# Kernel optimization log

Hardware: AMD Instinct MI355X
Metric: run time of the kernel (lower is better)

The kernel has to match this reference:

```python
import jax, jax.numpy as jnp
import numpy as np

B, T, D = 2, 2048, 2048
H, HD = 16, 128          # n_heads, head_dim (D = H * HD)
THETA = 10000.0
TOPK_RATIO = 0.55
EPS = 1e-5


def _ste(x, q):
    # straight-through estimator: forward = q, backward = identity
    return x + jax.lax.stop_gradient(q - x)


def ternary_weight(w):
    # absmean ternary quantization to {-1, 0, +1} * scale
    scale = jnp.mean(jnp.abs(w))
    wq = jnp.clip(jnp.round(w / (scale + EPS)), -1.0, 1.0) * scale
    return _ste(w, wq)


def quant_int(x, bits):
    # per-token (last-dim) absmax quantization to signed `bits`-bit grid
    qmax = 2.0 ** (bits - 1) - 1.0
    s = qmax / jnp.clip(jnp.max(jnp.abs(x), axis=-1, keepdims=True), EPS, None)
    q = jnp.clip(jnp.round(x * s), -qmax - 1.0, qmax) / s
    return _ste(x, q)


def topk_sparsify(x, ratio):
    # keep top-k values by magnitude per token, zero the rest
    d = x.shape[-1]
    k = max(1, int(ratio * d))
    flat = x.reshape(-1, d)
    _, idx = jax.lax.top_k(jnp.abs(flat), k)
    mask = jnp.zeros_like(flat).at[jnp.arange(flat.shape[0])[:, None], idx].set(1.0)
    return (flat * _ste(jnp.ones_like(flat), mask)).reshape(x.shape)


def bitlinear(x, w, act_mode):
    if act_mode == 'int4':
        x = quant_int(x, 4)
    elif act_mode == 'topk_int8':
        x = quant_int(topk_sparsify(x, TOPK_RATIO), 8)
    return x @ ternary_weight(w).T


def rope(x):
    # x: (B, H, T, hd); rotate-half RoPE with cat([freqs, freqs]) layout
    hd, t = x.shape[-1], x.shape[2]
    inv = 1.0 / THETA ** (jnp.arange(0, hd, 2, dtype=jnp.float32) / hd)
    freqs = jnp.arange(t, dtype=jnp.float32)[:, None] * inv[None, :]  # (T, hd/2)
    emb = jnp.concatenate([freqs, freqs], axis=-1)                     # (T, hd)
    cos = jnp.cos(emb)[None, None]
    sin = jnp.sin(emb)[None, None]
    x1, x2 = x[..., : hd // 2], x[..., hd // 2 :]
    rot = jnp.concatenate([-x2, x1], axis=-1)
    return x * cos + rot * sin


def setup_inputs() -> dict:
    key = jax.random.key(0)
    ks = jax.random.split(key, 5)
    return {
        'x': jax.random.normal(ks[0], (B, T, D), dtype=jnp.float32),
        'wq': jax.random.normal(ks[1], (D, D), dtype=jnp.float32) * 0.02,
        'wk': jax.random.normal(ks[2], (D, D), dtype=jnp.float32) * 0.02,
        'wv': jax.random.normal(ks[3], (D, D), dtype=jnp.float32) * 0.02,
        'wo': jax.random.normal(ks[4], (D, D), dtype=jnp.float32) * 0.02,
    }


def reference(x, wq, wk, wv, wo):
    b, t, _ = x.shape
    q = bitlinear(x, wq, 'int4').reshape(b, t, H, HD).transpose(0, 2, 1, 3)
    k = bitlinear(x, wk, 'int4').reshape(b, t, H, HD).transpose(0, 2, 1, 3)
    v = bitlinear(x, wv, 'int4').reshape(b, t, H, HD).transpose(0, 2, 1, 3)
    q = rope(q)
    k = rope(k)
    # bidirectional SDPA, no mask
    scores = jnp.einsum('bhqd,bhkd->bhqk', q, k) / jnp.sqrt(jnp.float32(HD))
    attn = jax.nn.softmax(scores, axis=-1)
    out = jnp.einsum('bhqk,bhkd->bhqd', attn, v)
    out = out.transpose(0, 2, 1, 3).reshape(b, t, H * HD)
    return bitlinear(out, wo, 'topk_int8')
```

## Files before the change

### kernel.cpp

```cpp
#include <hip/hip_runtime.h>
#include <stdint.h>
#include <math.h>


typedef __attribute__((ext_vector_type(8))) short short8;
typedef __attribute__((ext_vector_type(4))) int i32x4;
typedef __attribute__((ext_vector_type(8))) _Float16 f16x8;
typedef __attribute__((ext_vector_type(16))) float f32x16;

#define GLDS16(g, l)                                                        \
  __builtin_amdgcn_global_load_lds(                                         \
      (const __attribute__((address_space(1))) void*)(g),                   \
      (__attribute__((address_space(3))) void*)(l), 16, 0, 0)

__device__ __forceinline__ unsigned short f2bf(float v) {
  return (unsigned short)(__float_as_uint(v) >> 16);
}

__global__ __launch_bounds__(256) void k_costab(float* __restrict__ ct,
                                                float* __restrict__ st) {
  int idx = blockIdx.x * 256 + threadIdx.x;
  int t = idx >> 6, i = idx & 63;
  float f = (float)(2 * i) / 128.0f;
  float inv = 1.0f / powf(10000.0f, f);
  float fr = (float)t * inv;
  ct[idx] = cosf(fr);
  st[idx] = sinf(fr);
}

__global__ __launch_bounds__(256) void k_wsum(const float* __restrict__ w0,
                                              const float* __restrict__ w1,
                                              const float* __restrict__ w2,
                                              const float* __restrict__ w3,
                                              double* __restrict__ part) {
  int bx = blockIdx.x;
  int mat = bx >> 10;
  const float* w = (mat == 0) ? w0 : (mat == 1) ? w1 : (mat == 2) ? w2 : w3;
  int base = (bx & 1023) * 4096;
  double s = 0.0;
#pragma unroll
  for (int i = 0; i < 16; ++i)
    s += (double)fabsf(w[base + threadIdx.x + i * 256]);
  __shared__ double red[256];
  red[threadIdx.x] = s;
  __syncthreads();
  for (int off = 128; off; off >>= 1) {
    if (threadIdx.x < off) red[threadIdx.x] += red[threadIdx.x + off];
    __syncthreads();
  }
  if (threadIdx.x == 0) part[bx] = red[0];
}

__global__ __launch_bounds__(256) void k_wscale(const double* __restrict__ part,
                                                float* __restrict__ wsc) {
  int m = blockIdx.x, tid = threadIdx.x;
  const double* p = part + m * 1024;
  double s = p[tid] + p[tid + 256] + p[tid + 512] + p[tid + 768];
  __shared__ double red[256];
  red[tid] = s;
  __syncthreads();
  for (int off = 128; off; off >>= 1) {
    if (tid < off) red[tid] += red[tid + off];
    __syncthreads();
  }
  if (tid == 0) wsc[m] = (float)(red[0] / 4194304.0);
}

__global__ __launch_bounds__(256) void k_wquant(const float* __restrict__ w0,
                                                const float* __restrict__ w1,
                                                const float* __restrict__ w2,
                                                const float* __restrict__ w3,
                                                const float* __restrict__ wsc,
                                                signed char* __restrict__ wt) {
  int mat = blockIdx.y;
  const float* w = (mat == 0) ? w0 : (mat == 1) ? w1 : (mat == 2) ? w2 : w3;
  float se = wsc[mat] + 1e-5f;
  size_t base = (size_t)blockIdx.x * 4096;
  signed char* o = wt + (size_t)mat * 4194304 + base;
  const float* wp = w + base;
#pragma unroll 4
  for (int i = 0; i < 16; ++i) {
    int idx = threadIdx.x + i * 256;
    float v = rintf(wp[idx] / se);
    v = fminf(fmaxf(v, -1.0f), 1.0f);
    o[idx] = (signed char)v;
  }
}

__global__ __launch_bounds__(256) void k_xquant(const float* __restrict__ x,
                                                signed char* __restrict__ xq,
                                                float* __restrict__ sx) {
  int row = blockIdx.x, tid = threadIdx.x;
  const float* xr = x + (size_t)row * 2048;
  float v[8];
  float mx = 0.0f;
#pragma unroll
  for (int i = 0; i < 8; ++i) {
    v[i] = xr[tid + i * 256];
    mx = fmaxf(mx, fabsf(v[i]));
  }
  __shared__ float red[256];
  red[tid] = mx;
  __syncthreads();
  for (int off = 128; off; off >>= 1) {
    if (tid < off) red[tid] = fmaxf(red[tid], red[tid + off]);
    __syncthreads();
  }
  float s = 7.0f / fmaxf(red[0], 1e-5f);
#pragma unroll
  for (int i = 0; i < 8; ++i) {
    float q = rintf(v[i] * s);
    q = fminf(fmaxf(q, -8.0f), 7.0f);
    xq[(size_t)row * 2048 + tid + i * 256] = (signed char)q;
  }
  if (tid == 0) sx[row] = s;
}

__global__ __launch_bounds__(256) void k_gemm3(const signed char* __restrict__ A,
                                               const signed char* __restrict__ wtall,
                                               float* __restrict__ qo,
                                               float* __restrict__ vo,
                                               _Float16* __restrict__ khp,
                                               _Float16* __restrict__ klp,
                                               const float* __restrict__ srow,
                                               const float* __restrict__ wsc,
                                               const float* __restrict__ ct,
                                               const float* __restrict__ st) {
  __shared__ alignas(16) signed char As[128 * 64];
  __shared__ alignas(16) signed char Bs[128 * 64];
  __shared__ float fac[128];
  const int tid = threadIdx.x, wave = tid >> 6, lane = tid & 63;
  const int bxi = blockIdx.x;
  const int mat = bxi >> 4;
  const signed char* Bw = wtall + (size_t)mat * 4194304;
  const int brow = blockIdx.y * 128, bcol = (bxi & 15) * 128;
  if (tid < 128) fac[tid] = wsc[mat] / srow[brow + tid];
  const int wr = wave >> 1, wc = wave & 1;
  i32x4 acc[4][4];
#pragma unroll
  for (int m = 0; m < 4; ++m)
#pragma unroll
    for (int n = 0; n < 4; ++n) acc[m][n] = (i32x4){0, 0, 0, 0};
  const int srl = tid >> 2;
  const int ssw = ((tid & 3) ^ ((srl >> 1) & 3)) * 16;
  const signed char* Ag = A + (size_t)(brow + srl) * 2048 + ssw;
  const signed char* Bg = Bw + (size_t)(bcol + srl) * 2048 + ssw;
  char* AsB = (char*)As + wave * 1024;
  char* BsB = (char*)Bs + wave * 1024;
  const int fr = lane & 15, kb = lane >> 4;
  const int rsl = (kb ^ ((fr >> 1) & 3)) * 16;
  for (int k0 = 0; k0 < 2048; k0 += 64) {
    __syncthreads();
    GLDS16(Ag + k0, AsB);
    GLDS16(Ag + k0 + (size_t)64 * 2048, AsB + 4096);
    GLDS16(Bg + k0, BsB);
    GLDS16(Bg + k0 + (size_t)64 * 2048, BsB + 4096);
    __syncthreads();
    i32x4 af[4], bf[4];
#pragma unroll
    for (int m = 0; m < 4; ++m)
      af[m] = *(const i32x4*)&As[(wr * 64 + m * 16 + fr) * 64 + rsl];
#pragma unroll
    for (int n = 0; n < 4; ++n)
      bf[n] = *(const i32x4*)
           &Bs[(wc * 32 + (n & 1) * 16 + (n >> 1) * 64 + fr) * 64 + rsl];
#pragma unroll
    for (int m = 0; m < 4; ++m)
#pragma unroll
      for (int n = 0; n < 4; ++n)
        acc[m][n] = __builtin_amdgcn_mfma_i32_16x16x64_i8(af[m], bf[n],
                                                          acc[m][n], 0, 0, 0);
  }
  const int fq = lane >> 4;
  if (mat == 2) {
#pragma unroll
    for (int m = 0; m < 4; ++m)
#pragma unroll
      for (int n = 0; n < 4; ++n) {
        int col = bcol + wc * 32 + (n & 1) * 16 + (n >> 1) * 64 + fr;
#pragma unroll
        for (int r = 0; r < 4; ++r) {
          int row = wr * 64 + m * 16 + fq * 4 + r;
          vo[(size_t)(brow + row) * 2048 + col] = (float)acc[m][n][r] * fac[row];
        }
      }
  } else {
    const int hh = bcol >> 7;
#pragma unroll
    for (int m = 0; m < 4; ++m)
#pragma unroll
      for (int n = 0; n < 2; ++n) {
        int d1 = wc * 32 + n * 16 + fr;
#pragma unroll
        for (int r = 0; r < 4; ++r) {
          int row = wr * 64 + m * 16 + fq * 4 + r;
          int rg = brow + row;
          int t = rg & 2047, bb = rg >> 11;
          float c = ct[t * 64 + d1], sn = st[t * 64 + d1];
          float x1 = (float)acc[m][n][r] * fac[row];
          float x2 = (float)acc[m][n + 2][r] * fac[row];
          float y1 = x1 * c - x2 * sn;
          float y2 = x2 * c + x1 * sn;
          if (mat == 0) {
            qo[(size_t)rg * 2048 + bcol + d1] = y1;
            qo[(size_t)rg * 2048 + bcol + d1 + 64] = y2;
          } else {
            size_t ob = ((size_t)(bb * 16 + hh) * 2048 + t) * 128 + d1;
            _Float16 h1 = (_Float16)y1, h2 = (_Float16)y2;
            khp[ob] = h1;
            khp[ob + 64] = h2;
            klp[ob] = (_Float16)(y1 - (float)h1);
            klp[ob + 64] = (_Float16)(y2 - (float)h2);
          }
        }
      }
  }
}

__global__ __launch_bounds__(256) void k_gemm(const signed char* __restrict__ A,
                                              const signed char* __restrict__ Bw,
                                              float* __restrict__ C,
                                              const float* __restrict__ srow,
                                              const float* __restrict__ wsp) {
  __shared__ alignas(16) signed char As[128 * 64];
  __shared__ alignas(16) signed char Bs[128 * 64];
  __shared__ float fac[128];
  const int tid = threadIdx.x, wave = tid >> 6, lane = tid & 63;
  const int brow = blockIdx.y * 128, bcol = blockIdx.x * 128;
  if (tid < 128) fac[tid] = wsp[0] / srow[brow + tid];
  const int wr = wave >> 1, wc = wave & 1;
  i32x4 acc[4][4];
#pragma unroll
  for (int m = 0; m < 4; ++m)
#pragma unroll
    for (int n = 0; n < 4; ++n) acc[m][n] = (i32x4){0, 0, 0, 0};
  const int srl = tid >> 2;
  const int ssw = ((tid & 3) ^ ((srl >> 1) & 3)) * 16;
  const signed char* Ag = A + (size_t)(brow + srl) * 2048 + ssw;
  const signed char* Bg = Bw + (size_t)(bcol + srl) * 2048 + ssw;
  char* AsB = (char*)As + wave * 1024;
  char* BsB = (char*)Bs + wave * 1024;
  const int fr = lane & 15, kb = lane >> 4;
  const int rsl = (kb ^ ((fr >> 1) & 3)) * 16;
  for (int k0 = 0; k0 < 2048; k0 += 64) {
    __syncthreads();
    GLDS16(Ag + k0, AsB);
    GLDS16(Ag + k0 + (size_t)64 * 2048, AsB + 4096);
    GLDS16(Bg + k0, BsB);
    GLDS16(Bg + k0 + (size_t)64 * 2048, BsB + 4096);
    __syncthreads();
    i32x4 af[4], bf[4];
#pragma unroll
    for (int m = 0; m < 4; ++m)
      af[m] = *(const i32x4*)&As[(wr * 64 + m * 16 + fr) * 64 + rsl];
#pragma unroll
    for (int n = 0; n < 4; ++n)
      bf[n] = *(const i32x4*)&Bs[(wc * 64 + n * 16 + fr) * 64 + rsl];
#pragma unroll
    for (int m = 0; m < 4; ++m)
#pragma unroll
      for (int n = 0; n < 4; ++n)
        acc[m][n] = __builtin_amdgcn_mfma_i32_16x16x64_i8(af[m], bf[n],
                                                          acc[m][n], 0, 0, 0);
  }
  const int fq = lane >> 4;
#pragma unroll
  for (int m = 0; m < 4; ++m)
#pragma unroll
    for (int n = 0; n < 4; ++n)
#pragma unroll
      for (int r = 0; r < 4; ++r) {
        int row = wr * 64 + m * 16 + fq * 4 + r;
        C[(size_t)(brow + row) * 2048 + bcol + wc * 64 + n * 16 + fr] =
            (float)acc[m][n][r] * fac[row];
      }
}

__global__ __launch_bounds__(256) void k_vtrans(const float* __restrict__ vb,
                                                _Float16* __restrict__ vth,
                                                _Float16* __restrict__ vtl) {
  __shared__ float F[64][133];
  const int tid = threadIdx.x;
  const int bh = blockIdx.y, b = bh >> 4, h = bh & 15;
  const int t0 = blockIdx.x * 64;
  {
    const int tr = tid >> 2, tc = (tid & 3) * 32;
    const float* src = vb + ((size_t)(b * 2048 + t0 + tr)) * 2048 + h * 128 + tc;
#pragma unroll
    for (int j = 0; j < 8; ++j) {
      float4 v = *(const float4*)(src + j * 4);
      F[tr][tc + j * 4 + 0] = v.x;
      F[tr][tc + j * 4 + 1] = v.y;
      F[tr][tc + j * 4 + 2] = v.z;
      F[tr][tc + j * 4 + 3] = v.w;
    }
  }
  __syncthreads();
  {
    const int vd = tid >> 1, th = (tid & 1) * 32;
    f16x8 oh[4], ol[4];
#pragma unroll
    for (int j = 0; j < 32; ++j) {
      float x = F[th + j][vd];
      _Float16 hv = (_Float16)x;
      oh[j >> 3][j & 7] = hv;
      ol[j >> 3][j & 7] = (_Float16)(x - (float)hv);
    }
    _Float16* dh = vth + ((size_t)bh * 128 + vd) * 2048 + t0 + th;
    _Float16* dl = vtl + ((size_t)bh * 128 + vd) * 2048 + t0 + th;
#pragma unroll
    for (int j4 = 0; j4 < 4; ++j4) {
      *(f16x8*)(dh + j4 * 8) = oh[j4];
      *(f16x8*)(dl + j4 * 8) = ol[j4];
    }
  }
}

__global__ __launch_bounds__(256, 2) void k_attn(float* __restrict__ qb,
                                                 const _Float16* __restrict__ kh,
                                                 const _Float16* __restrict__ kl,
                                                 const _Float16* __restrict__ vth,
                                                 const _Float16* __restrict__ vtl) {
  __shared__ alignas(16) char KS[2][2][32 * 256];
  __shared__ alignas(16) char VS[2][2][128 * 64];
  const int tid = threadIdx.x;
  const int wave = tid >> 6, lane = tid & 63;
  const int rl = lane & 31, hi = lane >> 5, hi8 = hi * 8;
  const int bid = blockIdx.x;
  const int xcd = bid & 7, li = bid >> 3;
  const int bh = xcd * 4 + (li >> 4), qt = li & 15;
  const int b = bh >> 4, h = bh & 15;
  const size_t rowbase = (size_t)b * 2048;
  const int hcol = h * 128;
  const float F = 0.08838834764831845f * 1.44269504088896f;
  const float THR = 11.5415603f;

  f16x8 qh[8], ql[8];
  {
    const float* qsrc =
        qb + (rowbase + qt * 128 + wave * 32 + rl) * 2048 + hcol + hi8;
#pragma unroll
    for (int ds = 0; ds < 8; ++ds) {
      float4 a = *(const float4*)(qsrc + ds * 16);
      float4 c = *(const float4*)(qsrc + ds * 16 + 4);
      float v[8] = {a.x, a.y, a.z, a.w, c.x, c.y, c.z, c.w};
      f16x8 hh, ll;
#pragma unroll
      for (int i = 0; i < 8; ++i) {
        float sv = v[i] * F;
        _Float16 hv = (_Float16)sv;
        hh[i] = hv;
        ll[i] = (_Float16)(sv - (float)hv);
      }
      qh[ds] = hh;
      ql[ds] = ll;
    }
  }

  const int krl = lane >> 4, ksl = lane & 15;
  const int vrl = lane >> 2, vsl = lane & 3;
  size_t kofs[2], vofs[2];
#pragma unroll
  for (int i = 0; i < 2; ++i) {
    int krow = wave * 8 + i * 4 + krl;
    kofs[i] = (size_t)krow * 128 + ((ksl ^ (krow & 7)) << 3);
    int vrow = wave * 32 + i * 16 + vrl;
    vofs[i] = (size_t)vrow * 2048 + ((vsl ^ (vrow & 3)) << 3);
  }
  const _Float16* gkh = kh + (size_t)bh * 262144;
  const _Float16* gkl = kl + (size_t)bh * 262144;
  const _Float16* gvh = vth + (size_t)bh * 262144;
  const _Float16* gvl = vtl + (size_t)bh * 262144;

  f32x16 Oa[4];
#pragma unroll
  for (int df = 0; df < 4; ++df)
#pragma unroll
    for (int i = 0; i < 16; ++i) Oa[df][i] = 0.0f;
  float m = -INFINITY, lsum = 0.0f;

  {
#pragma unroll
    for (int i = 0; i < 2; ++i) {
      GLDS16(gkh + kofs[i], KS[0][0] + wave * 2048 + i * 1024);
      GLDS16(gkl + kofs[i], KS[0][1] + wave * 2048 + i * 1024);
      GLDS16(gvh + vofs[i], VS[0][0] + wave * 2048 + i * 1024);
      GLDS16(gvl + vofs[i], VS[0][1] + wave * 2048 + i * 1024);
    }
  }

  for (int kt = 0; kt < 64; ++kt) {
    const int bf = kt & 1;
    __syncthreads();
    if (kt < 63) {
      const _Float16* pkh = gkh + (size_t)(kt + 1) * 4096;
      const _Float16* pkl = gkl + (size_t)(kt + 1) * 4096;
      const _Float16* pvh = gvh + (size_t)(kt + 1) * 32;
      const _Float16* pvl = gvl + (size_t)(kt + 1) * 32;
      char* kd0 = KS[bf ^ 1][0] + wave * 2048;
      char* kd1 = KS[bf ^ 1][1] + wave * 2048;
      char* vd0 = VS[bf ^ 1][0] + wave * 2048;
      char* vd1 = VS[bf ^ 1][1] + wave * 2048;
#pragma unroll
      for (int i = 0; i < 2; ++i) {
        GLDS16(pkh + kofs[i], kd0 + i * 1024);
        GLDS16(pkl + kofs[i], kd1 + i * 1024);
        GLDS16(pvh + vofs[i], vd0 + i * 1024);
        GLDS16(pvl + vofs[i], vd1 + i * 1024);
      }
    }
    f32x16 sA = {}, sB = {}, sC = {};
    __builtin_amdgcn_s_setprio(1);
#pragma unroll
    for (int ds = 0; ds < 8; ++ds) {
      const int ra = rl * 256 + (((2 * ds + hi) ^ (rl & 7)) << 4);
      f16x8 ah = *(const f16x8*)(KS[bf][0] + ra);
      f16x8 al = *(const f16x8*)(KS[bf][1] + ra);
      sA = __builtin_amdgcn_mfma_f32_32x32x16_f16(ah, qh[ds], sA, 0, 0, 0);
      sB = __builtin_amdgcn_mfma_f32_32x32x16_f16(ah, ql[ds], sB, 0, 0, 0);
      sC = __builtin_amdgcn_mfma_f32_32x32x16_f16(al, qh[ds], sC, 0, 0, 0);
    }
    __builtin_amdgcn_s_setprio(0);
    f32x16 s;
#pragma unroll
    for (int i = 0; i < 16; ++i) s[i] = (sA[i] + sB[i]) + sC[i];
    float pm = fmaxf(
        fmaxf(fmaxf(fmaxf(s[0], s[1]), fmaxf(s[2], s[3])),
              fmaxf(fmaxf(s[4], s[5]), fmaxf(s[6], s[7]))),
        fmaxf(fmaxf(fmaxf(s[8], s[9]), fmaxf(s[10], s[11])),
              fmaxf(fmaxf(s[12], s[13]), fmaxf(s[14], s[15]))));
    pm = fmaxf(pm, __shfl_xor(pm, 32));
    float alpha = 1.0f;
    if (__any(pm > m + THR)) {
      float mn = fmaxf(m, pm);
      alpha = exp2f(m - mn);
      m = mn;
#pragma unroll
      for (int reg = 0; reg < 16; ++reg) {
        int qr = (reg & 3) + 8 * (reg >> 2) + 4 * hi;
        float av = __shfl(alpha, qr);
        Oa[0][reg] *= av;
        Oa[1][reg] *= av;
        Oa[2][reg] *= av;
        Oa[3][reg] *= av;
      }
    }
    unsigned int pkhh[4][2], pkll[4][2];
    float ls = 0.0f;
#pragma unroll
    for (int t4 = 0; t4 < 4; ++t4)
#pragma unroll
      for (int c2 = 0; c2 < 2; ++c2) {
        float pa = exp2f(s[4 * t4 + 2 * c2] - m);
        float pb = exp2f(s[4 * t4 + 2 * c2 + 1] - m);
        ls += pa + pb;
        auto hp = __builtin_amdgcn_cvt_pkrtz(pa, pb);
        float la = pa - (float)hp[0], lb = pb - (float)hp[1];
        auto lp = __builtin_amdgcn_cvt_pkrtz(la, lb);
        pkhh[t4][c2] = __builtin_bit_cast(unsigned int, hp);
        pkll[t4][c2] = __builtin_bit_cast(unsigned int, lp);
      }
    ls += __shfl_xor(ls, 32);
    lsum = lsum * alpha + ls;
    f16x8 paH[2], paL[2];
#pragma unroll
    for (int hf = 0; hf < 2; ++hf) {
      {
        unsigned int a0 = pkhh[2 * hf][0], b0 = pkhh[2 * hf + 1][0];
        unsigned int a1 = pkhh[2 * hf][1], b1 = pkhh[2 * hf + 1][1];
        asm("v_permlane32_swap_b32 %0, %1" : "+v"(a0), "+v"(b0));
        asm("v_permlane32_swap_b32 %0, %1" : "+v"(a1), "+v"(b1));
        uint4 u;
        u.x = a0; u.y = a1; u.z = b0; u.w = b1;
        paH[hf] = __builtin_bit_cast(f16x8, u);
      }
      {
        unsigned int a0 = pkll[2 * hf][0], b0 = pkll[2 * hf + 1][0];
        unsigned int a1 = pkll[2 * hf][1], b1 = pkll[2 * hf + 1][1];
        asm("v_permlane32_swap_b32 %0, %1" : "+v"(a0), "+v"(b0));
        asm("v_permlane32_swap_b32 %0, %1" : "+v"(a1), "+v"(b1));
        uint4 u;
        u.x = a0; u.y = a1; u.z = b0; u.w = b1;
        paL[hf] = __builtin_bit_cast(f16x8, u);
      }
    }
    __builtin_amdgcn_s_setprio(1);
#pragma unroll
    for (int df = 0; df < 4; ++df) {
#pragma unroll
      for (int hf = 0; hf < 2; ++hf) {
        const int va = (df * 32 + rl) * 64 + (((2 * hf + hi) ^ (rl & 3)) << 4);
        f16x8 vh = *(const f16x8*)(VS[bf][0] + va);
        f16x8 vl = *(const f16x8*)(VS[bf][1] + va);
        Oa[df] = __builtin_amdgcn_mfma_f32_32x32x16_f16(paH[hf], vh, Oa[df], 0, 0, 0);
        Oa[df] = __builtin_amdgcn_mfma_f32_32x32x16_f16(paH[hf], vl, Oa[df], 0, 0, 0);
        Oa[df] = __builtin_amdgcn_mfma_f32_32x32x16_f16(paL[hf], vh, Oa[df], 0, 0, 0);
      }
    }
    __builtin_amdgcn_s_setprio(0);
  }
  float linv = 1.0f / lsum;
  float* obase = qb + (rowbase + qt * 128 + wave * 32) * 2048 + hcol;
#pragma unroll
  for (int reg = 0; reg < 16; ++reg) {
    int qr = (reg & 3) + 8 * (reg >> 2) + 4 * hi;
    float lv = __shfl(linv, qr);
    float* orow = obase + (size_t)qr * 2048;
    orow[0 * 32 + rl] = Oa[0][reg] * lv;
    orow[1 * 32 + rl] = Oa[1][reg] * lv;
    orow[2 * 32 + rl] = Oa[2][reg] * lv;
    orow[3 * 32 + rl] = Oa[3][reg] * lv;
  }
}

__global__ __launch_bounds__(256) void k_topk(const float* __restrict__ ain,
                                              signed char* __restrict__ oq,
                                              float* __restrict__ so) {
  const int row = blockIdx.x, tid = threadIdx.x;
  const float* xr = ain + (size_t)row * 2048;
  __shared__ unsigned int bits[2048];
  __shared__ unsigned int hist[256];
  __shared__ unsigned int scn[256];
  __shared__ unsigned int stat[3];
#pragma unroll
  for (int j = 0; j < 8; ++j) {
    int i = tid * 8 + j;
    bits[i] = __float_as_uint(xr[i]) & 0x7fffffffu;
  }
  unsigned int mx = 0;
#pragma unroll
  for (int j = 0; j < 8; ++j) mx = max(mx, bits[tid * 8 + j]);
  scn[tid] = mx;
  __syncthreads();
  for (int off = 128; off; off >>= 1) {
    if (tid < off) scn[tid] = max(scn[tid], scn[tid + off]);
    __syncthreads();
  }
  if (tid == 0) { stat[0] = 0u; stat[1] = 1126u; stat[2] = scn[0]; }
  for (int p = 0; p < 4; ++p) {
    const int shift = 24 - 8 * p;
    hist[tid] = 0u;
    __syncthreads();
    unsigned int pref = stat[0];
    unsigned int rk0 = stat[1];
#pragma unroll
    for (int j = 0; j < 8; ++j) {
      unsigned int u = bits[tid * 8 + j];
      bool match = (p == 0) || ((u >> (shift + 8)) == pref);
      if (match) atomicAdd(&hist[(u >> shift) & 255u], 1u);
    }
    __syncthreads();
    scn[tid] = hist[tid];
    __syncthreads();
    for (int off = 1; off < 256; off <<= 1) {
      unsigned int v = (tid + off < 256) ? scn[tid + off] : 0u;
      __syncthreads();
      scn[tid] += v;
      __syncthreads();
    }
    unsigned int nxt = (tid == 255) ? 0u : scn[tid + 1];
    if (scn[tid] >= rk0 && nxt < rk0) {
      stat[0] = (pref << 8) | (unsigned int)tid;
      stat[1] = rk0 - nxt;
    }
    __syncthreads();
  }
  const unsigned int T = stat[0];
  const unsigned int rkeep = stat[1];
  const float rowmax = __uint_as_float(stat[2]);
  const float s = 127.0f / fmaxf(rowmax, 1e-5f);
  unsigned int cnt = 0;
#pragma unroll
  for (int j = 0; j < 8; ++j) cnt += (bits[tid * 8 + j] == T) ? 1u : 0u;
  scn[tid] = cnt;
  __syncthreads();
  for (int off = 1; off < 256; off <<= 1) {
    unsigned int v = (tid >= off) ? scn[tid - off] : 0u;
    __syncthreads();
    scn[tid] += v;
    __syncthreads();
  }
  unsigned int eqr = scn[tid] - cnt;
#pragma unroll
  for (int j = 0; j < 8; ++j) {
    int i = tid * 8 + j;
    unsigned int u = bits[i];
    bool keep = u > T;
    if (u == T) { keep = (eqr < rkeep); eqr++; }
    float q = 0.0f;
    if (keep) {
      q = rintf(xr[i] * s);
      q = fminf(fmaxf(q, -128.0f), 127.0f);
    }
    oq[(size_t)row * 2048 + i] = (signed char)q;
  }
  if (tid == 0) so[row] = s;
}

extern "C" void kernel_launch(void* const* d_in, const int* in_sizes, int n_in,
                              void* d_out, int out_size, void* d_ws,
                              size_t ws_size, hipStream_t stream) {
  const float* x = (const float*)d_in[0];
  const float* wq = (const float*)d_in[1];
  const float* wk = (const float*)d_in[2];
  const float* wv = (const float*)d_in[3];
  const float* wo = (const float*)d_in[4];
  float* out = (float*)d_out;

  char* ws = (char*)d_ws;
  size_t off = 0;
  auto alloc = [&](size_t bytes) -> void* {
    void* p = ws + off;
    off += (bytes + 255) & ~(size_t)255;
    return p;
  };
  signed char* wt = (signed char*)alloc(4ull * 2048 * 2048);
  signed char* xq = (signed char*)alloc(4096ull * 2048);
  float* qb = (float*)alloc(4096ull * 2048 * 4);
  float* vb = (float*)alloc(4096ull * 2048 * 4);
  _Float16* kh = (_Float16*)alloc(32ull * 2048 * 128 * 2);
  _Float16* kl = (_Float16*)alloc(32ull * 2048 * 128 * 2);
  _Float16* vth = (_Float16*)alloc(32ull * 128 * 2048 * 2);
  _Float16* vtl = (_Float16*)alloc(32ull * 128 * 2048 * 2);
  float* ct = (float*)alloc(2048ull * 64 * 4);
  float* st = (float*)alloc(2048ull * 64 * 4);
  float* sx = (float*)alloc(4096 * 4);
  float* so = (float*)alloc(4096 * 4);
  float* wsc = (float*)alloc(4 * 4);
  double* prt = (double*)alloc(4096 * 8);
  signed char* oq = (signed char*)vb;

  k_costab<<<512, 256, 0, stream>>>(ct, st);
  k_wsum<<<4096, 256, 0, stream>>>(wq, wk, wv, wo, prt);
  k_wscale<<<4, 256, 0, stream>>>(prt, wsc);
  k_wquant<<<dim3(1024, 4), 256, 0, stream>>>(wq, wk, wv, wo, wsc, wt);
  k_xquant<<<4096, 256, 0, stream>>>(x, xq, sx);

  k_gemm3<<<dim3(48, 32), 256, 0, stream>>>(xq, wt, qb, vb, kh, kl, sx, wsc,
                                            ct, st);
  k_vtrans<<<dim3(32, 32), 256, 0, stream>>>(vb, vth, vtl);
  k_attn<<<512, 256, 0, stream>>>(qb, kh, kl, vth, vtl);
  k_topk<<<4096, 256, 0, stream>>>(qb, oq, so);
  k_gemm<<<dim3(16, 32), 256, 0, stream>>>(oq, wt + 3ull * 4194304, out, so,
                                           wsc + 3);
}
```

Baseline: 442.3 us.

## Fuse V transpose into projection GEMM and software-pipeline attention PV step

The V projection epilogue now converts results to split fp16 hi/lo and writes them already transposed through shared memory, so the separate k_vtrans kernel and the fp32 V buffer round trip are no longer needed. In the attention kernel, the softmax and PV MFMAs for the previous key tile now run while the current tile's QK^T scores are computed. V tiles are loaded one iteration later, and a final drain step after the loop handles the last tile. This adds extra shared-memory syncs in the GEMM epilogue and keeps more scores live in registers, which may raise register pressure in the attention kernel.

```diff
diff --git a/kernel.cpp b/kernel.cpp
--- a/kernel.cpp
+++ b/kernel.cpp
@@ -119,9 +119,10 @@
 __global__ __launch_bounds__(256) void k_gemm3(const signed char* __restrict__ A,
                                                const signed char* __restrict__ wtall,
                                                float* __restrict__ qo,
-                                               float* __restrict__ vo,
                                                _Float16* __restrict__ khp,
                                                _Float16* __restrict__ klp,
+                                               _Float16* __restrict__ vth,
+                                               _Float16* __restrict__ vtl,
                                                const float* __restrict__ srow,
                                                const float* __restrict__ wsc,
                                                const float* __restrict__ ct,
@@ -172,20 +173,43 @@
                                                           acc[m][n], 0, 0, 0);
   }
   const int fq = lane >> 4;
+  const int hh = bcol >> 7;
+  const int bb0 = brow >> 11, tbase = brow & 2047;
   if (mat == 2) {
-#pragma unroll
-    for (int m = 0; m < 4; ++m)
-#pragma unroll
-      for (int n = 0; n < 4; ++n) {
-        int col = bcol + wc * 32 + (n & 1) * 16 + (n >> 1) * 64 + fr;
-#pragma unroll
-        for (int r = 0; r < 4; ++r) {
-          int row = wr * 64 + m * 16 + fq * 4 + r;
-          vo[(size_t)(brow + row) * 2048 + col] = (float)acc[m][n][r] * fac[row];
-        }
-      }
+    _Float16* Ah = (_Float16*)As;
+    _Float16* Al = (_Float16*)Bs;
+    const int bh = bb0 * 16 + hh;
+#pragma unroll
+    for (int q = 0; q < 4; ++q) {
+      __syncthreads();
+      if (wc == (q & 1)) {
+#pragma unroll
+        for (int m = 0; m < 4; ++m)
+#pragma unroll
+          for (int nn = 0; nn < 2; ++nn) {
+            int n = (q >> 1) * 2 + nn;
+            int dl = nn * 16 + fr;
+#pragma unroll
+            for (int r = 0; r < 4; ++r) {
+              int tl = wr * 64 + m * 16 + fq * 4 + r;
+              float val = (float)acc[m][n][r] * fac[tl];
+              _Float16 hv = (_Float16)val;
+              Ah[dl * 128 + tl] = hv;
+              Al[dl * 128 + tl] = (_Float16)(val - (float)hv);
+            }
+          }
+      }
+      __syncthreads();
+      {
+        int d = tid >> 3, tseg = (tid & 7) * 16;
+        size_t ob = ((size_t)bh * 128 + q * 32 + d) * 2048 + tbase + tseg;
+        *(f16x8*)(vth + ob) = *(const f16x8*)&Ah[d * 128 + tseg];
+        *(f16x8*)(vth + ob + 8) = *(const f16x8*)&Ah[d * 128 + tseg + 8];
+        *(f16x8*)(vtl + ob) = *(const f16x8*)&Al[d * 128 + tseg];
+        *(f16x8*)(vtl + ob + 8) = *(const f16x8*)&Al[d * 128 + tseg + 8];
+      }
+    }
   } else {
-    const int hh = bcol >> 7;
 #pragma unroll
     for (int m = 0; m < 4; ++m)
 #pragma unroll
@@ -195,7 +219,7 @@
         for (int r = 0; r < 4; ++r) {
           int row = wr * 64 + m * 16 + fq * 4 + r;
           int rg = brow + row;
-          int t = rg & 2047, bb = rg >> 11;
+          int t = rg & 2047;
           float c = ct[t * 64 + d1], sn = st[t * 64 + d1];
           float x1 = (float)acc[m][n][r] * fac[row];
           float x2 = (float)acc[m][n + 2][r] * fac[row];
@@ -205,7 +229,7 @@
             qo[(size_t)rg * 2048 + bcol + d1] = y1;
             qo[(size_t)rg * 2048 + bcol + d1 + 64] = y2;
           } else {
-            size_t ob = ((size_t)(bb * 16 + hh) * 2048 + t) * 128 + d1;
+            size_t ob = ((size_t)(bb0 * 16 + hh) * 2048 + t) * 128 + d1;
             _Float16 h1 = (_Float16)y1, h2 = (_Float16)y2;
             khp[ob] = h1;
             khp[ob + 64] = h2;
@@ -274,46 +298,6 @@
         C[(size_t)(brow + row) * 2048 + bcol + wc * 64 + n * 16 + fr] =
             (float)acc[m][n][r] * fac[row];
       }
-}
-
-__global__ __launch_bounds__(256) void k_vtrans(const float* __restrict__ vb,
-                                                _Float16* __restrict__ vth,
-                                                _Float16* __restrict__ vtl) {
-  __shared__ float F[64][133];
-  const int tid = threadIdx.x;
-  const int bh = blockIdx.y, b = bh >> 4, h = bh & 15;
-  const int t0 = blockIdx.x * 64;
-  {
-    const int tr = tid >> 2, tc = (tid & 3) * 32;
-    const float* src = vb + ((size_t)(b * 2048 + t0 + tr)) * 2048 + h * 128 + tc;
-#pragma unroll
-    for (int j = 0; j < 8; ++j) {
-      float4 v = *(const float4*)(src + j * 4);
-      F[tr][tc + j * 4 + 0] = v.x;
-      F[tr][tc + j * 4 + 1] = v.y;
-      F[tr][tc + j * 4 + 2] = v.z;
-      F[tr][tc + j * 4 + 3] = v.w;
-    }
-  }
-  __syncthreads();
-  {
-    const int vd = tid >> 1, th = (tid & 1) * 32;
-    f16x8 oh[4], ol[4];
-#pragma unroll
-    for (int j = 0; j < 32; ++j) {
-      float x = F[th + j][vd];
-      _Float16 hv = (_Float16)x;
-      oh[j >> 3][j & 7] = hv;
-      ol[j >> 3][j & 7] = (_Float16)(x - (float)hv);
-    }
-    _Float16* dh = vth + ((size_t)bh * 128 + vd) * 2048 + t0 + th;
-    _Float16* dl = vtl + ((size_t)bh * 128 + vd) * 2048 + t0 + th;
-#pragma unroll
-    for (int j4 = 0; j4 < 4; ++j4) {
-      *(f16x8*)(dh + j4 * 8) = oh[j4];
-      *(f16x8*)(dl + j4 * 8) = ol[j4];
-    }
-  }
 }
 
 __global__ __launch_bounds__(256, 2) void k_attn(float* __restrict__ qb,
@@ -378,15 +362,12 @@
 #pragma unroll
     for (int i = 0; i < 16; ++i) Oa[df][i] = 0.0f;
   float m = -INFINITY, lsum = 0.0f;
-
-  {
-#pragma unroll
-    for (int i = 0; i < 2; ++i) {
-      GLDS16(gkh + kofs[i], KS[0][0] + wave * 2048 + i * 1024);
-      GLDS16(gkl + kofs[i], KS[0][1] + wave * 2048 + i * 1024);
-      GLDS16(gvh + vofs[i], VS[0][0] + wave * 2048 + i * 1024);
-      GLDS16(gvl + vofs[i], VS[0][1] + wave * 2048 + i * 1024);
-    }
+  f32x16 sPrev;
+
+#pragma unroll
+  for (int i = 0; i < 2; ++i) {
+    GLDS16(gkh + kofs[i], KS[0][0] + wave * 2048 + i * 1024);
+    GLDS16(gkl + kofs[i], KS[0][1] + wave * 2048 + i * 1024);
   }
 
   for (int kt = 0; kt < 64; ++kt) {
@@ -395,16 +376,21 @@
     if (kt < 63) {
       const _Float16* pkh = gkh + (size_t)(kt + 1) * 4096;
       const _Float16* pkl = gkl + (size_t)(kt + 1) * 4096;
-      const _Float16* pvh = gvh + (size_t)(kt + 1) * 32;
-      const _Float16* pvl = gvl + (size_t)(kt + 1) * 32;
       char* kd0 = KS[bf ^ 1][0] + wave * 2048;
       char* kd1 = KS[bf ^ 1][1] + wave * 2048;
-      char* vd0 = VS[bf ^ 1][0] + wave * 2048;
-      char* vd1 = VS[bf ^ 1][1] + wave * 2048;
 #pragma unroll
       for (int i = 0; i < 2; ++i) {
         GLDS16(pkh + kofs[i], kd0 + i * 1024);
         GLDS16(pkl + kofs[i], kd1 + i * 1024);
+      }
+    }
+    {
+      const _Float16* pvh = gvh + (size_t)kt * 32;
+      const _Float16* pvl = gvl + (size_t)kt * 32;
+      char* vd0 = VS[bf][0] + wave * 2048;
+      char* vd1 = VS[bf][1] + wave * 2048;
+#pragma unroll
+      for (int i = 0; i < 2; ++i) {
         GLDS16(pvh + vofs[i], vd0 + i * 1024);
         GLDS16(pvl + vofs[i], vd1 + i * 1024);
       }
@@ -421,14 +407,96 @@
       sC = __builtin_amdgcn_mfma_f32_32x32x16_f16(al, qh[ds], sC, 0, 0, 0);
     }
     __builtin_amdgcn_s_setprio(0);
-    f32x16 s;
-#pragma unroll
-    for (int i = 0; i < 16; ++i) s[i] = (sA[i] + sB[i]) + sC[i];
+    if (kt > 0) {
+      const int pbf = (kt - 1) & 1;
+      float pm = fmaxf(
+          fmaxf(fmaxf(fmaxf(sPrev[0], sPrev[1]), fmaxf(sPrev[2], sPrev[3])),
+                fmaxf(fmaxf(sPrev[4], sPrev[5]), fmaxf(sPrev[6], sPrev[7]))),
+          fmaxf(fmaxf(fmaxf(sPrev[8], sPrev[9]), fmaxf(sPrev[10], sPrev[11])),
+                fmaxf(fmaxf(sPrev[12], sPrev[13]),
+                      fmaxf(sPrev[14], sPrev[15]))));
+      pm = fmaxf(pm, __shfl_xor(pm, 32));
+      float alpha = 1.0f;
+      if (__any(pm > m + THR)) {
+        float mn = fmaxf(m, pm);
+        alpha = exp2f(m - mn);
+        m = mn;
+#pragma unroll
+        for (int reg = 0; reg < 16; ++reg) {
+          int qr = (reg & 3) + 8 * (reg >> 2) + 4 * hi;
+          float av = __shfl(alpha, qr);
+          Oa[0][reg] *= av;
+          Oa[1][reg] *= av;
+          Oa[2][reg] *= av;
+          Oa[3][reg] *= av;
+        }
+      }
+      unsigned int pkhh[4][2], pkll[4][2];
+      float ls = 0.0f;
+#pragma unroll
+      for (int t4 = 0; t4 < 4; ++t4)
+#pragma unroll
+        for (int c2 = 0; c2 < 2; ++c2) {
+          float pa = exp2f(sPrev[4 * t4 + 2 * c2] - m);
+          float pb = exp2f(sPrev[4 * t4 + 2 * c2 + 1] - m);
+          ls += pa + pb;
+          auto hp = __builtin_amdgcn_cvt_pkrtz(pa, pb);
+          float la = pa - (float)hp[0], lb = pb - (float)hp[1];
+          auto lp = __builtin_amdgcn_cvt_pkrtz(la, lb);
+          pkhh[t4][c2] = __builtin_bit_cast(unsigned int, hp);
+          pkll[t4][c2] = __builtin_bit_cast(unsigned int, lp);
+        }
+      ls += __shfl_xor(ls, 32);
+      lsum = lsum * alpha + ls;
+      f16x8 paH[2], paL[2];
+#pragma unroll
+      for (int hf = 0; hf < 2; ++hf) {
+        {
+          unsigned int a0 = pkhh[2 * hf][0], b0 = pkhh[2 * hf + 1][0];
+          unsigned int a1 = pkhh[2 * hf][1], b1 = pkhh[2 * hf + 1][1];
+          asm("v_permlane32_swap_b32 %0, %1" : "+v"(a0), "+v"(b0));
+          asm("v_permlane32_swap_b32 %0, %1" : "+v"(a1), "+v"(b1));
+          uint4 u;
+          u.x = a0; u.y = a1; u.z = b0; u.w = b1;
+          paH[hf] = __builtin_bit_cast(f16x8, u);
+        }
+        {
+          unsigned int a0 = pkll[2 * hf][0], b0 = pkll[2 * hf + 1][0];
+          unsigned int a1 = pkll[2 * hf][1], b1 = pkll[2 * hf + 1][1];
+          asm("v_permlane32_swap_b32 %0, %1" : "+v"(a0), "+v"(b0));
+          asm("v_permlane32_swap_b32 %0, %1" : "+v"(a1), "+v"(b1));
+          uint4 u;
+          u.x = a0; u.y = a1; u.z = b0; u.w = b1;
+          paL[hf] = __builtin_bit_cast(f16x8, u);
+        }
+      }
+      __builtin_amdgcn_s_setprio(1);
+#pragma unroll
+      for (int df = 0; df < 4; ++df) {
+#pragma unroll
+        for (int hf = 0; hf < 2; ++hf) {
+          const int va =
+              (df * 32 + rl) * 64 + (((2 * hf + hi) ^ (rl & 3)) << 4);
+          f16x8 vh = *(const f16x8*)(VS[pbf][0] + va);
+          f16x8 vl = *(const f16x8*)(VS[pbf][1] + va);
+          Oa[df] = __builtin_amdgcn_mfma_f32_32x32x16_f16(paH[hf], vh, Oa[df], 0, 0, 0);
+          Oa[df] = __builtin_amdgcn_mfma_f32_32x32x16_f16(paH[hf], vl, Oa[df], 0, 0, 0);
+          Oa[df] = __builtin_amdgcn_mfma_f32_32x32x16_f16(paL[hf], vh, Oa[df], 0, 0, 0);
+        }
+      }
+      __builtin_amdgcn_s_setprio(0);
+    }
+#pragma unroll
+    for (int i = 0; i < 16; ++i) sPrev[i] = (sA[i] + sB[i]) + sC[i];
+  }
+  __syncthreads();
+  {
     float pm = fmaxf(
-        fmaxf(fmaxf(fmaxf(s[0], s[1]), fmaxf(s[2], s[3])),
-              fmaxf(fmaxf(s[4], s[5]), fmaxf(s[6], s[7]))),
-        fmaxf(fmaxf(fmaxf(s[8], s[9]), fmaxf(s[10], s[11])),
-              fmaxf(fmaxf(s[12], s[13]), fmaxf(s[14], s[15]))));
+        fmaxf(fmaxf(fmaxf(sPrev[0], sPrev[1]), fmaxf(sPrev[2], sPrev[3])),
+              fmaxf(fmaxf(sPrev[4], sPrev[5]), fmaxf(sPrev[6], sPrev[7]))),
+        fmaxf(fmaxf(fmaxf(sPrev[8], sPrev[9]), fmaxf(sPrev[10], sPrev[11])),
+              fmaxf(fmaxf(sPrev[12], sPrev[13]),
+                    fmaxf(sPrev[14], sPrev[15]))));
     pm = fmaxf(pm, __shfl_xor(pm, 32));
     float alpha = 1.0f;
     if (__any(pm > m + THR)) {
@@ -451,8 +519,8 @@
     for (int t4 = 0; t4 < 4; ++t4)
 #pragma unroll
       for (int c2 = 0; c2 < 2; ++c2) {
-        float pa = exp2f(s[4 * t4 + 2 * c2] - m);
-        float pb = exp2f(s[4 * t4 + 2 * c2 + 1] - m);
+        float pa = exp2f(sPrev[4 * t4 + 2 * c2] - m);
+        float pb = exp2f(sPrev[4 * t4 + 2 * c2 + 1] - m);
         ls += pa + pb;
         auto hp = __builtin_amdgcn_cvt_pkrtz(pa, pb);
         float la = pa - (float)hp[0], lb = pb - (float)hp[1];
@@ -484,20 +552,18 @@
         paL[hf] = __builtin_bit_cast(f16x8, u);
       }
     }
-    __builtin_amdgcn_s_setprio(1);
 #pragma unroll
     for (int df = 0; df < 4; ++df) {
 #pragma unroll
       for (int hf = 0; hf < 2; ++hf) {
         const int va = (df * 32 + rl) * 64 + (((2 * hf + hi) ^ (rl & 3)) << 4);
-        f16x8 vh = *(const f16x8*)(VS[bf][0] + va);
-        f16x8 vl = *(const f16x8*)(VS[bf][1] + va);
+        f16x8 vh = *(const f16x8*)(VS[1][0] + va);
+        f16x8 vl = *(const f16x8*)(VS[1][1] + va);
         Oa[df] = __builtin_amdgcn_mfma_f32_32x32x16_f16(paH[hf], vh, Oa[df], 0, 0, 0);
         Oa[df] = __builtin_amdgcn_mfma_f32_32x32x16_f16(paH[hf], vl, Oa[df], 0, 0, 0);
         Oa[df] = __builtin_amdgcn_mfma_f32_32x32x16_f16(paL[hf], vh, Oa[df], 0, 0, 0);
       }
     }
-    __builtin_amdgcn_s_setprio(0);
   }
   float linv = 1.0f / lsum;
   float* obase = qb + (rowbase + qt * 128 + wave * 32) * 2048 + hcol;
@@ -617,7 +683,7 @@
   signed char* wt = (signed char*)alloc(4ull * 2048 * 2048);
   signed char* xq = (signed char*)alloc(4096ull * 2048);
   float* qb = (float*)alloc(4096ull * 2048 * 4);
-  float* vb = (float*)alloc(4096ull * 2048 * 4);
+  signed char* oq = (signed char*)alloc(4096ull * 2048);
   _Float16* kh = (_Float16*)alloc(32ull * 2048 * 128 * 2);
   _Float16* kl = (_Float16*)alloc(32ull * 2048 * 128 * 2);
   _Float16* vth = (_Float16*)alloc(32ull * 128 * 2048 * 2);
@@ -628,7 +694,6 @@
   float* so = (float*)alloc(4096 * 4);
   float* wsc = (float*)alloc(4 * 4);
   double* prt = (double*)alloc(4096 * 8);
-  signed char* oq = (signed char*)vb;
 
   k_costab<<<512, 256, 0, stream>>>(ct, st);
   k_wsum<<<4096, 256, 0, stream>>>(wq, wk, wv, wo, prt);
@@ -636,9 +701,8 @@
   k_wquant<<<dim3(1024, 4), 256, 0, stream>>>(wq, wk, wv, wo, wsc, wt);
   k_xquant<<<4096, 256, 0, stream>>>(x, xq, sx);
 
-  k_gemm3<<<dim3(48, 32), 256, 0, stream>>>(xq, wt, qb, vb, kh, kl, sx, wsc,
-                                            ct, st);
-  k_vtrans<<<dim3(32, 32), 256, 0, stream>>>(vb, vth, vtl);
+  k_gemm3<<<dim3(48, 32), 256, 0, stream>>>(xq, wt, qb, kh, kl, vth, vtl, sx,
+                                            wsc, ct, st);
   k_attn<<<512, 256, 0, stream>>>(qb, kh, kl, vth, vtl);
   k_topk<<<4096, 256, 0, stream>>>(qb, oq, so);
   k_gemm<<<dim3(16, 32), 256, 0, stream>>>(oq, wt + 3ull * 4194304, out, so,
```

Result: faster. 428.2 us (-3.2%).

## Fuse V transpose into QKV GEMM and split attention over KV halves

Applied to the files above, without the earlier changes.

The V projection epilogue now writes transposed hi/lo fp16 V through shared memory, so the separate k_vtrans kernel and the fp32 V buffer are gone. Attention is split into two KV halves per query tile (1024 blocks, single-buffered LDS, higher occupancy bound). Each half writes unnormalised partial outputs plus m/l, and a new combine kernel merges them. This trades the removed transpose pass and the extra parallelism against extra partial-output traffic, a combine launch, and the loss of double-buffered K/V prefetch.

```diff
diff --git a/kernel.cpp b/kernel.cpp
--- a/kernel.cpp
+++ b/kernel.cpp
@@ -119,9 +119,10 @@
 __global__ __launch_bounds__(256) void k_gemm3(const signed char* __restrict__ A,
                                                const signed char* __restrict__ wtall,
                                                float* __restrict__ qo,
-                                               float* __restrict__ vo,
                                                _Float16* __restrict__ khp,
                                                _Float16* __restrict__ klp,
+                                               _Float16* __restrict__ vth,
+                                               _Float16* __restrict__ vtl,
                                                const float* __restrict__ srow,
                                                const float* __restrict__ wsc,
                                                const float* __restrict__ ct,
@@ -172,20 +173,43 @@
                                                           acc[m][n], 0, 0, 0);
   }
   const int fq = lane >> 4;
+  const int hh = bcol >> 7;
+  const int bb0 = brow >> 11, tbase = brow & 2047;
   if (mat == 2) {
-#pragma unroll
-    for (int m = 0; m < 4; ++m)
-#pragma unroll
-      for (int n = 0; n < 4; ++n) {
-        int col = bcol + wc * 32 + (n & 1) * 16 + (n >> 1) * 64 + fr;
-#pragma unroll
-        for (int r = 0; r < 4; ++r) {
-          int row = wr * 64 + m * 16 + fq * 4 + r;
-          vo[(size_t)(brow + row) * 2048 + col] = (float)acc[m][n][r] * fac[row];
-        }
-      }
+    _Float16* Ah = (_Float16*)As;
+    _Float16* Al = (_Float16*)Bs;
+    const int bh = bb0 * 16 + hh;
+#pragma unroll
+    for (int q = 0; q < 4; ++q) {
+      __syncthreads();
+      if (wc == (q & 1)) {
+#pragma unroll
+        for (int m = 0; m < 4; ++m)
+#pragma unroll
+          for (int nn = 0; nn < 2; ++nn) {
+            int n = (q >> 1) * 2 + nn;
+            int dl = nn * 16 + fr;
+#pragma unroll
+            for (int r = 0; r < 4; ++r) {
+              int tl = wr * 64 + m * 16 + fq * 4 + r;
+              float val = (float)acc[m][n][r] * fac[tl];
+              _Float16 hv = (_Float16)val;
+              Ah[dl * 128 + tl] = hv;
+              Al[dl * 128 + tl] = (_Float16)(val - (float)hv);
+            }
+          }
+      }
+      __syncthreads();
+      {
+        int d = tid >> 3, tseg = (tid & 7) * 16;
+        size_t ob = ((size_t)bh * 128 + q * 32 + d) * 2048 + tbase + tseg;
+        *(f16x8*)(vth + ob) = *(const f16x8*)&Ah[d * 128 + tseg];
+        *(f16x8*)(vth + ob + 8) = *(const f16x8*)&Ah[d * 128 + tseg + 8];
+        *(f16x8*)(vtl + ob) = *(const f16x8*)&Al[d * 128 + tseg];
+        *(f16x8*)(vtl + ob + 8) = *(const f16x8*)&Al[d * 128 + tseg + 8];
+      }
+    }
   } else {
-    const int hh = bcol >> 7;
 #pragma unroll
     for (int m = 0; m < 4; ++m)
 #pragma unroll
@@ -195,7 +219,7 @@
         for (int r = 0; r < 4; ++r) {
           int row = wr * 64 + m * 16 + fq * 4 + r;
           int rg = brow + row;
-          int t = rg & 2047, bb = rg >> 11;
+          int t = rg & 2047;
           float c = ct[t * 64 + d1], sn = st[t * 64 + d1];
           float x1 = (float)acc[m][n][r] * fac[row];
           float x2 = (float)acc[m][n + 2][r] * fac[row];
@@ -205,7 +229,7 @@
             qo[(size_t)rg * 2048 + bcol + d1] = y1;
             qo[(size_t)rg * 2048 + bcol + d1 + 64] = y2;
           } else {
-            size_t ob = ((size_t)(bb * 16 + hh) * 2048 + t) * 128 + d1;
+            size_t ob = ((size_t)(bb0 * 16 + hh) * 2048 + t) * 128 + d1;
             _Float16 h1 = (_Float16)y1, h2 = (_Float16)y2;
             khp[ob] = h1;
             khp[ob + 64] = h2;
@@ -276,59 +300,23 @@
       }
 }
 
-__global__ __launch_bounds__(256) void k_vtrans(const float* __restrict__ vb,
-                                                _Float16* __restrict__ vth,
-                                                _Float16* __restrict__ vtl) {
-  __shared__ float F[64][133];
-  const int tid = threadIdx.x;
-  const int bh = blockIdx.y, b = bh >> 4, h = bh & 15;
-  const int t0 = blockIdx.x * 64;
-  {
-    const int tr = tid >> 2, tc = (tid & 3) * 32;
-    const float* src = vb + ((size_t)(b * 2048 + t0 + tr)) * 2048 + h * 128 + tc;
-#pragma unroll
-    for (int j = 0; j < 8; ++j) {
-      float4 v = *(const float4*)(src + j * 4);
-      F[tr][tc + j * 4 + 0] = v.x;
-      F[tr][tc + j * 4 + 1] = v.y;
-      F[tr][tc + j * 4 + 2] = v.z;
-      F[tr][tc + j * 4 + 3] = v.w;
-    }
-  }
-  __syncthreads();
-  {
-    const int vd = tid >> 1, th = (tid & 1) * 32;
-    f16x8 oh[4], ol[4];
-#pragma unroll
-    for (int j = 0; j < 32; ++j) {
-      float x = F[th + j][vd];
-      _Float16 hv = (_Float16)x;
-      oh[j >> 3][j & 7] = hv;
-      ol[j >> 3][j & 7] = (_Float16)(x - (float)hv);
-    }
-    _Float16* dh = vth + ((size_t)bh * 128 + vd) * 2048 + t0 + th;
-    _Float16* dl = vtl + ((size_t)bh * 128 + vd) * 2048 + t0 + th;
-#pragma unroll
-    for (int j4 = 0; j4 < 4; ++j4) {
-      *(f16x8*)(dh + j4 * 8) = oh[j4];
-      *(f16x8*)(dl + j4 * 8) = ol[j4];
-    }
-  }
-}
-
-__global__ __launch_bounds__(256, 2) void k_attn(float* __restrict__ qb,
+__global__ __launch_bounds__(256, 4) void k_attn(const float* __restrict__ qb,
                                                  const _Float16* __restrict__ kh,
                                                  const _Float16* __restrict__ kl,
                                                  const _Float16* __restrict__ vth,
-                                                 const _Float16* __restrict__ vtl) {
-  __shared__ alignas(16) char KS[2][2][32 * 256];
-  __shared__ alignas(16) char VS[2][2][128 * 64];
+                                                 const _Float16* __restrict__ vtl,
+                                                 float* __restrict__ Op,
+                                                 float* __restrict__ ml) {
+  __shared__ alignas(16) char KS[2][32 * 256];
+  __shared__ alignas(16) char VS[2][128 * 64];
   const int tid = threadIdx.x;
   const int wave = tid >> 6, lane = tid & 63;
   const int rl = lane & 31, hi = lane >> 5, hi8 = hi * 8;
   const int bid = blockIdx.x;
   const int xcd = bid & 7, li = bid >> 3;
-  const int bh = xcd * 4 + (li >> 4), qt = li & 15;
+  const int bh = xcd * 4 + (li >> 5);
+  const int qt = (li & 31) >> 1;
+  const int sp = li & 1;
   const int b = bh >> 4, h = bh & 15;
   const size_t rowbase = (size_t)b * 2048;
   const int hcol = h * 128;
@@ -365,12 +353,12 @@
     int krow = wave * 8 + i * 4 + krl;
     kofs[i] = (size_t)krow * 128 + ((ksl ^ (krow & 7)) << 3);
     int vrow = wave * 32 + i * 16 + vrl;
-    vofs[i] = (size_t)vrow * 2048 + ((vsl ^ (vrow & 3)) << 3);
-  }
-  const _Float16* gkh = kh + (size_t)bh * 262144;
-  const _Float16* gkl = kl + (size_t)bh * 262144;
-  const _Float16* gvh = vth + (size_t)bh * 262144;
-  const _Float16* gvl = vtl + (size_t)bh * 262144;
+    vofs[i] = (size_t)vrow * 2048 + ((vsl ^ ((vrow >> 1) & 3)) << 3);
+  }
+  const _Float16* gkh = kh + (size_t)bh * 262144 + (size_t)sp * 32 * 4096;
+  const _Float16* gkl = kl + (size_t)bh * 262144 + (size_t)sp * 32 * 4096;
+  const _Float16* gvh = vth + (size_t)bh * 262144 + (size_t)sp * 32 * 32;
+  const _Float16* gvl = vtl + (size_t)bh * 262144 + (size_t)sp * 32 * 32;
 
   f32x16 Oa[4];
 #pragma unroll
@@ -379,43 +367,23 @@
     for (int i = 0; i < 16; ++i) Oa[df][i] = 0.0f;
   float m = -INFINITY, lsum = 0.0f;
 
-  {
-#pragma unroll
-    for (int i = 0; i < 2; ++i) {
-      GLDS16(gkh + kofs[i], KS[0][0] + wave * 2048 + i * 1024);
-      GLDS16(gkl + kofs[i], KS[0][1] + wave * 2048 + i * 1024);
-      GLDS16(gvh + vofs[i], VS[0][0] + wave * 2048 + i * 1024);
-      GLDS16(gvl + vofs[i], VS[0][1] + wave * 2048 + i * 1024);
-    }
-  }
-
-  for (int kt = 0; kt < 64; ++kt) {
-    const int bf = kt & 1;
-    __syncthreads();
-    if (kt < 63) {
-      const _Float16* pkh = gkh + (size_t)(kt + 1) * 4096;
-      const _Float16* pkl = gkl + (size_t)(kt + 1) * 4096;
-      const _Float16* pvh = gvh + (size_t)(kt + 1) * 32;
-      const _Float16* pvl = gvl + (size_t)(kt + 1) * 32;
-      char* kd0 = KS[bf ^ 1][0] + wave * 2048;
-      char* kd1 = KS[bf ^ 1][1] + wave * 2048;
-      char* vd0 = VS[bf ^ 1][0] + wave * 2048;
-      char* vd1 = VS[bf ^ 1][1] + wave * 2048;
-#pragma unroll
-      for (int i = 0; i < 2; ++i) {
-        GLDS16(pkh + kofs[i], kd0 + i * 1024);
-        GLDS16(pkl + kofs[i], kd1 + i * 1024);
-        GLDS16(pvh + vofs[i], vd0 + i * 1024);
-        GLDS16(pvl + vofs[i], vd1 + i * 1024);
-      }
-    }
+#pragma unroll
+  for (int i = 0; i < 2; ++i) {
+    GLDS16(gkh + kofs[i], KS[0] + wave * 2048 + i * 1024);
+    GLDS16(gkl + kofs[i], KS[1] + wave * 2048 + i * 1024);
+    GLDS16(gvh + vofs[i], VS[0] + wave * 2048 + i * 1024);
+    GLDS16(gvl + vofs[i], VS[1] + wave * 2048 + i * 1024);
+  }
+
+  for (int kt = 0; kt < 32; ++kt) {
+    __syncthreads();
     f32x16 sA = {}, sB = {}, sC = {};
     __builtin_amdgcn_s_setprio(1);
 #pragma unroll
     for (int ds = 0; ds < 8; ++ds) {
       const int ra = rl * 256 + (((2 * ds + hi) ^ (rl & 7)) << 4);
-      f16x8 ah = *(const f16x8*)(KS[bf][0] + ra);
-      f16x8 al = *(const f16x8*)(KS[bf][1] + ra);
+      f16x8 ah = *(const f16x8*)(KS[0] + ra);
+      f16x8 al = *(const f16x8*)(KS[1] + ra);
       sA = __builtin_amdgcn_mfma_f32_32x32x16_f16(ah, qh[ds], sA, 0, 0, 0);
       sB = __builtin_amdgcn_mfma_f32_32x32x16_f16(ah, ql[ds], sB, 0, 0, 0);
       sC = __builtin_amdgcn_mfma_f32_32x32x16_f16(al, qh[ds], sC, 0, 0, 0);
@@ -489,28 +457,63 @@
     for (int df = 0; df < 4; ++df) {
 #pragma unroll
       for (int hf = 0; hf < 2; ++hf) {
-        const int va = (df * 32 + rl) * 64 + (((2 * hf + hi) ^ (rl & 3)) << 4);
-        f16x8 vh = *(const f16x8*)(VS[bf][0] + va);
-        f16x8 vl = *(const f16x8*)(VS[bf][1] + va);
+        const int va =
+            (df * 32 + rl) * 64 + (((2 * hf + hi) ^ ((rl >> 1) & 3)) << 4);
+        f16x8 vh = *(const f16x8*)(VS[0] + va);
+        f16x8 vl = *(const f16x8*)(VS[1] + va);
         Oa[df] = __builtin_amdgcn_mfma_f32_32x32x16_f16(paH[hf], vh, Oa[df], 0, 0, 0);
         Oa[df] = __builtin_amdgcn_mfma_f32_32x32x16_f16(paH[hf], vl, Oa[df], 0, 0, 0);
         Oa[df] = __builtin_amdgcn_mfma_f32_32x32x16_f16(paL[hf], vh, Oa[df], 0, 0, 0);
       }
     }
     __builtin_amdgcn_s_setprio(0);
-  }
-  float linv = 1.0f / lsum;
-  float* obase = qb + (rowbase + qt * 128 + wave * 32) * 2048 + hcol;
+    __syncthreads();
+    if (kt < 31) {
+      const _Float16* pkh = gkh + (size_t)(kt + 1) * 4096;
+      const _Float16* pkl = gkl + (size_t)(kt + 1) * 4096;
+      const _Float16* pvh = gvh + (size_t)(kt + 1) * 32;
+      const _Float16* pvl = gvl + (size_t)(kt + 1) * 32;
+#pragma unroll
+      for (int i = 0; i < 2; ++i) {
+        GLDS16(pkh + kofs[i], KS[0] + wave * 2048 + i * 1024);
+        GLDS16(pkl + kofs[i], KS[1] + wave * 2048 + i * 1024);
+        GLDS16(pvh + vofs[i], VS[0] + wave * 2048 + i * 1024);
+        GLDS16(pvl + vofs[i], VS[1] + wave * 2048 + i * 1024);
+      }
+    }
+  }
+  const size_t prow = ((size_t)sp * 32 + bh) * 2048 + qt * 128 + wave * 32;
+  float* obase = Op + prow * 128;
 #pragma unroll
   for (int reg = 0; reg < 16; ++reg) {
     int qr = (reg & 3) + 8 * (reg >> 2) + 4 * hi;
-    float lv = __shfl(linv, qr);
-    float* orow = obase + (size_t)qr * 2048;
-    orow[0 * 32 + rl] = Oa[0][reg] * lv;
-    orow[1 * 32 + rl] = Oa[1][reg] * lv;
-    orow[2 * 32 + rl] = Oa[2][reg] * lv;
-    orow[3 * 32 + rl] = Oa[3][reg] * lv;
-  }
+    float* orow = obase + (size_t)qr * 128;
+    orow[0 * 32 + rl] = Oa[0][reg];
+    orow[1 * 32 + rl] = Oa[1][reg];
+    orow[2 * 32 + rl] = Oa[2][reg];
+    orow[3 * 32 + rl] = Oa[3][reg];
+  }
+  if (hi == 0) {
+    ml[(prow + rl) * 2] = m;
+    ml[(prow + rl) * 2 + 1] = lsum;
+  }
+}
+
+__global__ __launch_bounds__(256) void k_comb(const float* __restrict__ Op,
+                                              const float* __restrict__ ml,
+                                              float* __restrict__ qb) {
+  const int tid = threadIdx.x;
+  const int row = blockIdx.x * 2 + (tid >> 7);
+  const int d = tid & 127;
+  const size_t r1 = (size_t)row, r2 = (size_t)row + 65536;
+  float m1 = ml[r1 * 2], l1 = ml[r1 * 2 + 1];
+  float m2 = ml[r2 * 2], l2 = ml[r2 * 2 + 1];
+  float M = fmaxf(m1, m2);
+  float a1 = exp2f(m1 - M), a2 = exp2f(m2 - M);
+  float o = a1 * Op[r1 * 128 + d] + a2 * Op[r2 * 128 + d];
+  float l = a1 * l1 + a2 * l2;
+  int bh = row >> 11, t = row & 2047;
+  qb[((size_t)(bh >> 4) * 2048 + t) * 2048 + (bh & 15) * 128 + d] = o / l;
 }
 
 __global__ __launch_bounds__(256) void k_topk(const float* __restrict__ ain,
@@ -617,18 +620,19 @@
   signed char* wt = (signed char*)alloc(4ull * 2048 * 2048);
   signed char* xq = (signed char*)alloc(4096ull * 2048);
   float* qb = (float*)alloc(4096ull * 2048 * 4);
-  float* vb = (float*)alloc(4096ull * 2048 * 4);
+  signed char* oq = (signed char*)alloc(4096ull * 2048);
   _Float16* kh = (_Float16*)alloc(32ull * 2048 * 128 * 2);
   _Float16* kl = (_Float16*)alloc(32ull * 2048 * 128 * 2);
   _Float16* vth = (_Float16*)alloc(32ull * 128 * 2048 * 2);
   _Float16* vtl = (_Float16*)alloc(32ull * 128 * 2048 * 2);
+  float* Opart = (float*)alloc(2ull * 65536 * 128 * 4);
+  float* mlb = (float*)alloc(2ull * 65536 * 2 * 4);
   float* ct = (float*)alloc(2048ull * 64 * 4);
   float* st = (float*)alloc(2048ull * 64 * 4);
   float* sx = (float*)alloc(4096 * 4);
   float* so = (float*)alloc(4096 * 4);
   float* wsc = (float*)alloc(4 * 4);
   double* prt = (double*)alloc(4096 * 8);
-  signed char* oq = (signed char*)vb;
 
   k_costab<<<512, 256, 0, stream>>>(ct, st);
   k_wsum<<<4096, 256, 0, stream>>>(wq, wk, wv, wo, prt);
@@ -636,10 +640,10 @@
   k_wquant<<<dim3(1024, 4), 256, 0, stream>>>(wq, wk, wv, wo, wsc, wt);
   k_xquant<<<4096, 256, 0, stream>>>(x, xq, sx);
 
-  k_gemm3<<<dim3(48, 32), 256, 0, stream>>>(xq, wt, qb, vb, kh, kl, sx, wsc,
-                                            ct, st);
-  k_vtrans<<<dim3(32, 32), 256, 0, stream>>>(vb, vth, vtl);
-  k_attn<<<512, 256, 0, stream>>>(qb, kh, kl, vth, vtl);
+  k_gemm3<<<dim3(48, 32), 256, 0, stream>>>(xq, wt, qb, kh, kl, vth, vtl, sx,
+                                            wsc, ct, st);
+  k_attn<<<1024, 256, 0, stream>>>(qb, kh, kl, vth, vtl, Opart, mlb);
+  k_comb<<<32768, 256, 0, stream>>>(Opart, mlb, qb);
   k_topk<<<4096, 256, 0, stream>>>(qb, oq, so);
   k_gemm<<<dim3(16, 32), 256, 0, stream>>>(oq, wt + 3ull * 4194304, out, so,
                                            wsc + 3);
```

Measured after the change: 838.0 us. +89.5%, slower.
